# Performance work log

Hardware: AMD Instinct MI355X
Metric: run time of the kernel (lower is better)

The kernel has to match this reference:

```python
import jax, jax.numpy as jnp
import numpy as np

LEVEL_SHAPES = [(100, 134), (50, 67), (25, 34), (13, 17)]  # (H, W) per feature level
NH, NL, NP, D, DFF = 8, 4, 4, 256, 1024
DH = D // NH
LTOT = sum(h * w for h, w in LEVEL_SHAPES)  # 17821
BS, NQ = 4, 300


def _ln(x, w, b):
    m = x.mean(-1, keepdims=True)
    v = ((x - m) ** 2).mean(-1, keepdims=True)
    return (x - m) / jnp.sqrt(v + 1e-5) * w + b


def _mha(q, k, v, in_w, in_b, out_w, out_b):
    B, N, _ = q.shape
    wq, wk, wv = jnp.split(in_w, 3, axis=0)
    bq, bk, bv = jnp.split(in_b, 3)
    qh = (q @ wq.T + bq).reshape(B, N, NH, DH)
    kh = (k @ wk.T + bk).reshape(B, N, NH, DH)
    vh = (v @ wv.T + bv).reshape(B, N, NH, DH)
    a = jax.nn.softmax(jnp.einsum('bqhd,bkhd->bhqk', qh, kh) / float(np.sqrt(DH)), axis=-1)
    o = jnp.einsum('bhqk,bkhd->bqhd', a, vh).reshape(B, N, D)
    return o @ out_w.T + out_b


def _bilinear(img, grid):
    # img [B,C,H,W]; grid [B,N,2] in [-1,1]; align_corners=False, zero padding
    B, C, H, W = img.shape
    x = (grid[..., 0] + 1.0) * 0.5 * W - 0.5
    y = (grid[..., 1] + 1.0) * 0.5 * H - 0.5
    x0f = jnp.floor(x); y0f = jnp.floor(y)
    wx = x - x0f; wy = y - y0f
    x0 = x0f.astype(jnp.int32); y0 = y0f.astype(jnp.int32)
    flat = img.reshape(B, C, H * W)

    def gather(xi, yi):
        m = ((xi >= 0) & (xi < W) & (yi >= 0) & (yi < H)).astype(img.dtype)
        idx = jnp.clip(yi, 0, H - 1) * W + jnp.clip(xi, 0, W - 1)
        g = jnp.take_along_axis(flat, jnp.broadcast_to(idx[:, None, :], (B, C, idx.shape[-1])), axis=2)
        return g * m[:, None, :]

    return (gather(x0, y0) * ((1 - wx) * (1 - wy))[:, None]
            + gather(x0 + 1, y0) * (wx * (1 - wy))[:, None]
            + gather(x0, y0 + 1) * ((1 - wx) * wy)[:, None]
            + gather(x0 + 1, y0 + 1) * (wx * wy)[:, None])


def _msdeform(value, loc, aw):
    # value [B,L,NH,DH]; loc [B,Nq,NH,NL,NP,2] in [0,1]; aw [B,Nq,NH,NL,NP]
    B, Nq = loc.shape[0], loc.shape[1]
    outs = []
    start = 0
    for l, (Hl, Wl) in enumerate(LEVEL_SHAPES):
        v = value[:, start:start + Hl * Wl].transpose(0, 2, 3, 1).reshape(B * NH, DH, Hl, Wl)
        g = (2.0 * loc[:, :, :, l] - 1.0).transpose(0, 2, 1, 3, 4).reshape(B * NH, Nq * NP, 2)
        outs.append(_bilinear(v, g).reshape(B * NH, DH, Nq, NP))
        start += Hl * Wl
    samp = jnp.stack(outs, axis=3)  # [B*NH, DH, Nq, NL, NP]
    w = aw.transpose(0, 2, 1, 3, 4).reshape(B * NH, 1, Nq, NL, NP)
    out = (samp * w).sum(axis=(3, 4))  # [B*NH, DH, Nq]
    return out.reshape(B, NH, DH, Nq).transpose(0, 3, 1, 2).reshape(B, Nq, D)


def _deform_branch(q, ref, src_other, vw, vb, ow, ob, aww, awb, outw, outb):
    B, Nq, _ = q.shape
    value = (src_other @ vw.T + vb).reshape(B, -1, NH, DH)
    off = (q @ ow.T + ob).reshape(B, Nq, NH, NL, NP, 2)
    aw = jax.nn.softmax((q @ aww.T + awb).reshape(B, Nq, NH, NL * NP), axis=-1).reshape(B, Nq, NH, NL, NP)
    norm = jnp.array([[w, h] for h, w in LEVEL_SHAPES], dtype=q.dtype)  # (W,H) per level
    loc = ref[:, :, None, :, None, :] + off / norm[None, None, None, :, None, :]
    return _msdeform(value, loc, aw) @ outw.T + outb


def reference(tgt_RGB, tgt_T, query_pos_RGB, query_pos_T, ref_RGB, ref_T, src_RGB, src_T,
              sa_in_w, sa_in_b, sa_out_w, sa_out_b, ln_w, ln_b,
              ffn_w1, ffn_b1, ffn_w2, ffn_b2,
              val_w, val_b, off_w, off_b, aw_w, aw_b, cout_w, cout_b):
    # --- dual self-attention (eval mode: dropout = identity) ---
    q_RGB = tgt_RGB + query_pos_RGB
    q_T = tgt_T + query_pos_T
    sa_RGB = _mha(q_RGB, q_RGB, tgt_RGB, sa_in_w[0], sa_in_b[0], sa_out_w[0], sa_out_b[0])
    sa_T = _mha(q_T, q_T, tgt_T, sa_in_w[1], sa_in_b[1], sa_out_w[1], sa_out_b[1])
    tgt_RGB = _ln(tgt_RGB + sa_RGB, ln_w[0, 1], ln_b[0, 1])  # norm2_RGB
    tgt_T = _ln(tgt_T + sa_T, ln_w[1, 1], ln_b[1, 1])        # norm2_T
    # --- interactive multi-scale deformable cross-attn: RGB queries sample T memory & vice versa ---
    qc_RGB = tgt_RGB + query_pos_RGB
    qc_T = tgt_T + query_pos_T
    t2_RGB = _deform_branch(qc_RGB, ref_RGB, src_T, val_w[0], val_b[0], off_w[0], off_b[0], aw_w[0], aw_b[0], cout_w[0], cout_b[0])
    t2_T = _deform_branch(qc_T, ref_T, src_RGB, val_w[1], val_b[1], off_w[1], off_b[1], aw_w[1], aw_b[1], cout_w[1], cout_b[1])
    F_RGB, F_T = t2_RGB, t2_T
    # cross residuals exactly as in the torch layer (note the modality swap)
    r = tgt_T + t2_RGB
    t = r + t2_T
    tgt_RGB = _ln(r, ln_w[0, 0], ln_b[0, 0])  # norm1_RGB
    tgt_T = _ln(t, ln_w[1, 0], ln_b[1, 0])    # norm1_T
    # --- FFNs ---
    tgt_RGB = _ln(tgt_RGB + (jax.nn.relu(tgt_RGB @ ffn_w1[0].T + ffn_b1[0]) @ ffn_w2[0].T + ffn_b2[0]), ln_w[0, 2], ln_b[0, 2])
    tgt_T = _ln(tgt_T + (jax.nn.relu(tgt_T @ ffn_w1[1].T + ffn_b1[1]) @ ffn_w2[1].T + ffn_b2[1]), ln_w[1, 2], ln_b[1, 2])
    return tgt_RGB, tgt_T, F_RGB, F_T


def setup_inputs() -> dict:
    key = jax.random.key(0)
    ks = jax.random.split(key, 24)
    s = 0.05
    w = lambda k, shp: jax.random.normal(k, shp, dtype=jnp.float32) * s
    return {
        'tgt_RGB': jax.random.normal(ks[0], (BS, NQ, D), jnp.float32),
        'tgt_T': jax.random.normal(ks[1], (BS, NQ, D), jnp.float32),
        'query_pos_RGB': jax.random.normal(ks[2], (BS, NQ, D), jnp.float32),
        'query_pos_T': jax.random.normal(ks[3], (BS, NQ, D), jnp.float32),
        'ref_RGB': jax.random.uniform(ks[4], (BS, NQ, NL, 2), jnp.float32),
        'ref_T': jax.random.uniform(ks[5], (BS, NQ, NL, 2), jnp.float32),
        'src_RGB': jax.random.normal(ks[6], (BS, LTOT, D), jnp.float32),
        'src_T': jax.random.normal(ks[7], (BS, LTOT, D), jnp.float32),
        'sa_in_w': w(ks[8], (2, 3 * D, D)),
        'sa_in_b': jnp.zeros((2, 3 * D), jnp.float32),
        'sa_out_w': w(ks[9], (2, D, D)),
        'sa_out_b': jnp.zeros((2, D), jnp.float32),
        'ln_w': jnp.ones((2, 3, D), jnp.float32),
        'ln_b': jnp.zeros((2, 3, D), jnp.float32),
        'ffn_w1': w(ks[10], (2, DFF, D)),
        'ffn_b1': jnp.zeros((2, DFF), jnp.float32),
        'ffn_w2': w(ks[11], (2, D, DFF)),
        'ffn_b2': jnp.zeros((2, D), jnp.float32),
        'val_w': w(ks[12], (2, D, D)),
        'val_b': jnp.zeros((2, D), jnp.float32),
        'off_w': w(ks[13], (2, NH * NL * NP * 2, D)),
        'off_b': jax.random.normal(ks[14], (2, NH * NL * NP * 2), jnp.float32) * 0.5,
        'aw_w': w(ks[15], (2, NH * NL * NP, D)),
        'aw_b': jnp.zeros((2, NH * NL * NP), jnp.float32),
        'cout_w': w(ks[16], (2, D, D)),
        'cout_b': jnp.zeros((2, D), jnp.float32),
    }
```

## Files before the change

kernel.cpp:

```cpp
#include <hip/hip_runtime.h>
#include <hip/hip_bf16.h>
#include <cstddef>
#include <math.h>

#define NTOK 1200
#define LTOT_C 17821
#define MVAL 71284
#define STOK (NTOK * 256)

typedef __attribute__((ext_vector_type(8))) short bhalf8;
typedef __attribute__((ext_vector_type(4))) float f32x4;

static __device__ __forceinline__ short f2bf(float f) {
    unsigned u = __builtin_bit_cast(unsigned, f);
    u += 0x7fffu + ((u >> 16) & 1u);
    return (short)(u >> 16);
}
static __device__ __forceinline__ float bf2f(short s) {
    unsigned u = ((unsigned)(unsigned short)s) << 16;
    return __builtin_bit_cast(float, u);
}
static __device__ __forceinline__ bhalf8 cvt8(float4 a, float4 b) {
    bhalf8 h;
    h[0] = f2bf(a.x); h[1] = f2bf(a.y); h[2] = f2bf(a.z); h[3] = f2bf(a.w);
    h[4] = f2bf(b.x); h[5] = f2bf(b.y); h[6] = f2bf(b.z); h[7] = f2bf(b.w);
    return h;
}
static __device__ __forceinline__ void gload_lds16(const void* g, void* l) {
    __builtin_amdgcn_global_load_lds(
        (const __attribute__((address_space(1))) void*)g,
        (__attribute__((address_space(3))) void*)l, 16, 0, 0);
}

struct WcvtArgs { const float* s[10]; short* d[10]; int n[10]; };
__global__ __launch_bounds__(256) void wcvt(WcvtArgs a) {
    const int ti = blockIdx.y;
    const float* s = a.s[ti];
    short* d = a.d[ti];
    const int n = a.n[ti];
    for (int base = (blockIdx.x * 256 + threadIdx.x) * 8; base < n; base += gridDim.x * 256 * 8) {
        const float4 f0 = *reinterpret_cast<const float4*>(s + base);
        const float4 f1 = *reinterpret_cast<const float4*>(s + base + 4);
        *reinterpret_cast<bhalf8*>(d + base) = cvt8(f0, f1);
    }
}

__global__ __launch_bounds__(256) void prep_act(
    const float* __restrict__ tgt0, const float* __restrict__ tgt1,
    const float* __restrict__ pos0, const float* __restrict__ pos1,
    short* __restrict__ qb_bf, short* __restrict__ tgtb,
    const float* __restrict__ off_b, const float* __restrict__ aw_b,
    float* __restrict__ baw)
{
    const int z = blockIdx.y;
    if (blockIdx.x == 0 && z == 0) {
        for (int i = threadIdx.x; i < 768; i += 256) {
            const int zz = i / 384, j = i - zz * 384;
            baw[i] = (j < 256) ? off_b[zz * 256 + j] : aw_b[zz * 128 + (j - 256)];
        }
    }
    const float* tg = z ? tgt1 : tgt0;
    const float* ps = z ? pos1 : pos0;
    const int base = (blockIdx.x * 256 + threadIdx.x) * 8;
    if (base >= STOK) return;
    const float4 t0 = *reinterpret_cast<const float4*>(tg + base);
    const float4 t1 = *reinterpret_cast<const float4*>(tg + base + 4);
    const float4 p0 = *reinterpret_cast<const float4*>(ps + base);
    const float4 p1 = *reinterpret_cast<const float4*>(ps + base + 4);
    float4 s0 = make_float4(t0.x + p0.x, t0.y + p0.y, t0.z + p0.z, t0.w + p0.w);
    float4 s1 = make_float4(t1.x + p1.x, t1.y + p1.y, t1.z + p1.z, t1.w + p1.w);
    *reinterpret_cast<bhalf8*>(qb_bf + (size_t)z * STOK + base) = cvt8(s0, s1);
    *reinterpret_cast<bhalf8*>(tgtb + (size_t)z * STOK + base) = cvt8(t0, t1);
}

__global__ __launch_bounds__(256) void gemm_val(
    const float* __restrict__ A0, const float* __restrict__ A1,
    const short* __restrict__ Wbf, const float* __restrict__ bias,
    short* __restrict__ C)
{
    __shared__ alignas(16) short As[64 * 64];
    __shared__ alignas(16) short Bs[2][128 * 64];
    const int i = blockIdx.x;
    const int widx = (i & 7) * 557 + (i >> 3);
    const int x = widx & 1;
    const int yz = widx >> 1;
    const int z = yz / 1114;
    const int y = yz - z * 1114;
    const float* A = z ? A1 : A0;
    const short* W = Wbf + (size_t)z * 65536;
    const float* bz = bias + z * 256;
    short* Cz = C + (size_t)z * MVAL * 256;
    const int t = threadIdx.x;
    const int wave = t >> 6, lane = t & 63;
    const int l15 = lane & 15, l4 = lane >> 4;
    const int wr = wave >> 1, wc = wave & 1;
    const int bm = y * 64, bn = x * 128;
    f32x4 acc[2][4] = {};

    const int nr8 = lane >> 3, q8 = lane & 7;
    auto stageW = [&](int k0, int buf) {
        #pragma unroll
        for (int ii = 0; ii < 4; ++ii) {
            const int c = wave * 4 + ii;
            const int n = c * 8 + nr8;
            gload_lds16(W + (size_t)(bn + n) * 256 + k0 + ((q8 ^ nr8) << 3),
                        (char*)&Bs[buf][0] + c * 1024);
        }
    };
    float4 paf[2][2];
    auto issueA = [&](int k0) {
        #pragma unroll
        for (int ii = 0; ii < 2; ++ii) {
            const int G = t + ii * 256;
            const int m = G >> 3, g = G & 7;
            const int row = min(bm + m, MVAL - 1);
            const float* s = A + (size_t)row * 256 + k0 + g * 8;
            paf[ii][0] = *reinterpret_cast<const float4*>(s);
            paf[ii][1] = *reinterpret_cast<const float4*>(s + 4);
        }
    };
    auto commitA = [&]() {
        #pragma unroll
        for (int ii = 0; ii < 2; ++ii) {
            const int G = t + ii * 256;
            const int m = G >> 3, g = G & 7;
            *reinterpret_cast<bhalf8*>(&As[m * 64 + ((g ^ (m & 7)) << 3)]) =
                cvt8(paf[ii][0], paf[ii][1]);
        }
    };
    auto compute = [&](int wbuf) {
        #pragma unroll
        for (int kf = 0; kf < 2; ++kf) {
            bhalf8 af[2], bfv[4];
            #pragma unroll
            for (int mf = 0; mf < 2; ++mf) {
                const int m = wr * 32 + (mf << 4) + l15;
                const int g = ((kf << 2) + l4) ^ (m & 7);
                af[mf] = *reinterpret_cast<const bhalf8*>(&As[m * 64 + (g << 3)]);
            }
            #pragma unroll
            for (int nf = 0; nf < 4; ++nf) {
                const int n = (wc << 6) + (nf << 4) + l15;
                const int g = ((kf << 2) + l4) ^ (n & 7);
                bfv[nf] = *reinterpret_cast<const bhalf8*>(&Bs[wbuf][n * 64 + (g << 3)]);
            }
            #pragma unroll
            for (int mf = 0; mf < 2; ++mf)
                #pragma unroll
                for (int nf = 0; nf < 4; ++nf)
                    acc[mf][nf] = __builtin_amdgcn_mfma_f32_16x16x32_bf16(
                        af[mf], bfv[nf], acc[mf][nf], 0, 0, 0);
        }
    };

    issueA(0);
    stageW(0, 0);
    commitA();
    __syncthreads();
    #pragma unroll
    for (int ks = 0; ks < 4; ++ks) {
        const int cur = ks & 1, nxt = cur ^ 1;
        if (ks + 1 < 4) {
            issueA((ks + 1) << 6);
            stageW((ks + 1) << 6, nxt);
        }
        compute(cur);
        if (ks + 1 < 4) {
            __syncthreads();
            commitA();
            __syncthreads();
        }
    }

    float br[4];
    #pragma unroll
    for (int nf = 0; nf < 4; ++nf) br[nf] = bz[bn + (wc << 6) + (nf << 4) + l15];
    #pragma unroll
    for (int mf = 0; mf < 2; ++mf) {
        #pragma unroll
        for (int j = 0; j < 4; ++j) {
            const int row = bm + wr * 32 + (mf << 4) + (l4 << 2) + j;
            if (row >= MVAL) continue;
            const int colbase = bn + (wc << 6);
            #pragma unroll
            for (int nf = 0; nf < 4; ++nf)
                Cz[(size_t)row * 256 + colbase + (nf << 4) + l15] = f2bf(acc[mf][nf][j] + br[nf]);
        }
    }
}

template<bool HASRES, bool RELU, bool OUT_BF16, int BM, int NK>
__global__ __launch_bounds__(256) void gemm_bf16(
    const short* __restrict__ Av, size_t aStrideZ, int lda,
    const short* __restrict__ Wv, size_t wStrideZ, int ldw,
    const float* __restrict__ bias, size_t biasStrideZ,
    const float* __restrict__ Res0, const float* __restrict__ Res1, int ldr,
    void* __restrict__ Cv, size_t cStrideZ, int ldc,
    int M)
{
    constexpr int MFR = BM / 32;
    constexpr int ACW = BM / 32;
    __shared__ alignas(16) short As[2][BM * 64];
    __shared__ alignas(16) short Bs[2][128 * 64];
    const int z = blockIdx.z;
    const short* W = Wv + (size_t)z * wStrideZ;
    const float* bz = bias + (size_t)z * biasStrideZ;
    const int t = threadIdx.x;
    const int wave = t >> 6, lane = t & 63;
    const int l15 = lane & 15, l4 = lane >> 4;
    const int wr = wave >> 1, wc = wave & 1;
    const int bm = blockIdx.y * BM, bn = blockIdx.x * 128;
    f32x4 acc[MFR][4] = {};

    const int nr8 = lane >> 3, q8 = lane & 7;
    auto stageW = [&](int k0, int buf) {
        #pragma unroll
        for (int i = 0; i < 4; ++i) {
            const int c = wave * 4 + i;
            const int n = c * 8 + nr8;
            gload_lds16(W + (size_t)(bn + n) * ldw + k0 + ((q8 ^ nr8) << 3),
                        (char*)&Bs[buf][0] + c * 1024);
        }
    };
    auto stageA = [&](int k0, int buf) {
        #pragma unroll
        for (int i = 0; i < ACW; ++i) {
            const int c = wave * ACW + i;
            const int m = c * 8 + nr8;
            const int row = min(bm + m, M - 1);
            gload_lds16(Av + (size_t)z * aStrideZ + (size_t)row * lda + k0 + ((q8 ^ (m & 7)) << 3),
                        (char*)&As[buf][0] + c * 1024);
        }
    };
    auto compute = [&](int buf) {
        #pragma unroll
        for (int kf = 0; kf < 2; ++kf) {
            bhalf8 af[MFR], bfv[4];
            #pragma unroll
            for (int mf = 0; mf < MFR; ++mf) {
                const int m = wr * (BM / 2) + (mf << 4) + l15;
                const int g = ((kf << 2) + l4) ^ (m & 7);
                af[mf] = *reinterpret_cast<const bhalf8*>(&As[buf][m * 64 + (g << 3)]);
            }
            #pragma unroll
            for (int nf = 0; nf < 4; ++nf) {
                const int n = (wc << 6) + (nf << 4) + l15;
                const int g = ((kf << 2) + l4) ^ (n & 7);
                bfv[nf] = *reinterpret_cast<const bhalf8*>(&Bs[buf][n * 64 + (g << 3)]);
            }
            #pragma unroll
            for (int mf = 0; mf < MFR; ++mf)
                #pragma unroll
                for (int nf = 0; nf < 4; ++nf)
                    acc[mf][nf] = __builtin_amdgcn_mfma_f32_16x16x32_bf16(
                        af[mf], bfv[nf], acc[mf][nf], 0, 0, 0);
        }
    };

    stageA(0, 0);
    stageW(0, 0);
    __syncthreads();
    #pragma unroll
    for (int ks = 0; ks < NK; ++ks) {
        const int cur = ks & 1, nxt = cur ^ 1;
        if (ks + 1 < NK) {
            stageA((ks + 1) << 6, nxt);
            stageW((ks + 1) << 6, nxt);
        }
        compute(cur);
        __syncthreads();
    }

    const float* Rz = HASRES ? (z ? Res1 : Res0) : nullptr;
    float br[4];
    #pragma unroll
    for (int nf = 0; nf < 4; ++nf) br[nf] = bz[bn + (wc << 6) + (nf << 4) + l15];
    #pragma unroll
    for (int mf = 0; mf < MFR; ++mf) {
        #pragma unroll
        for (int j = 0; j < 4; ++j) {
            const int row = bm + wr * (BM / 2) + (mf << 4) + (l4 << 2) + j;
            if (row >= M) continue;
            const int colbase = bn + (wc << 6);
            #pragma unroll
            for (int nf = 0; nf < 4; ++nf) {
                const int col = colbase + (nf << 4) + l15;
                float v = acc[mf][nf][j] + br[nf];
                if (HASRES) v += Rz[(size_t)row * ldr + col];
                if (RELU) v = fmaxf(v, 0.f);
                if (OUT_BF16)
                    ((short*)Cv + (size_t)z * cStrideZ)[(size_t)row * ldc + col] = f2bf(v);
                else
                    ((float*)Cv + (size_t)z * cStrideZ)[(size_t)row * ldc + col] = v;
            }
        }
    }
}

__global__ __launch_bounds__(256) void attn2_kernel(
    const float* __restrict__ qkv_base, short* __restrict__ out_base)
{
    const float scale = 0.17677669529663687f;
    const float* qkv = qkv_base + (size_t)blockIdx.z * 921600;
    short* outp = out_base + (size_t)blockIdx.z * STOK;
    const int b = blockIdx.y >> 3, h = blockIdx.y & 7;
    const int t = threadIdx.x;
    const int ql = t & 31;
    const int kg = t >> 5;
    const int q = blockIdx.x * 32 + ql;
    const bool act = q < 300;
    const float* base = qkv + (size_t)b * 300 * 768;

    float qreg[32];
    if (act) {
        const float4* qp = reinterpret_cast<const float4*>(base + (size_t)q * 768 + h * 32);
        #pragma unroll
        for (int d4 = 0; d4 < 8; ++d4) {
            const float4 v = qp[d4];
            qreg[d4 * 4 + 0] = v.x; qreg[d4 * 4 + 1] = v.y;
            qreg[d4 * 4 + 2] = v.z; qreg[d4 * 4 + 3] = v.w;
        }
    }
    __shared__ float Ks[64][32];
    __shared__ float Vs[64][32];
    float m = -1e30f, l = 0.f, o[32];
    #pragma unroll
    for (int d = 0; d < 32; ++d) o[d] = 0.f;

    for (int k0 = 0; k0 < 300; k0 += 64) {
        const int cnt = min(64, 300 - k0);
        __syncthreads();
        for (int i = t; i < cnt * 32; i += 256) {
            const int kr = i >> 5, d = i & 31;
            Ks[kr][d] = base[(size_t)(k0 + kr) * 768 + 256 + h * 32 + d];
            Vs[kr][d] = base[(size_t)(k0 + kr) * 768 + 512 + h * 32 + d];
        }
        __syncthreads();
        if (act) {
            for (int kk = kg; kk < cnt; kk += 8) {
                const float4* krow = reinterpret_cast<const float4*>(&Ks[kk][0]);
                float s = 0.f;
                #pragma unroll
                for (int d4 = 0; d4 < 8; ++d4) {
                    const float4 kv = krow[d4];
                    s += qreg[d4 * 4 + 0] * kv.x + qreg[d4 * 4 + 1] * kv.y
                       + qreg[d4 * 4 + 2] * kv.z + qreg[d4 * 4 + 3] * kv.w;
                }
                s *= scale;
                const float4* vrow = reinterpret_cast<const float4*>(&Vs[kk][0]);
                if (s <= m) {
                    const float e = __expf(s - m);
                    l += e;
                    #pragma unroll
                    for (int d4 = 0; d4 < 8; ++d4) {
                        const float4 vv = vrow[d4];
                        o[d4 * 4 + 0] += e * vv.x; o[d4 * 4 + 1] += e * vv.y;
                        o[d4 * 4 + 2] += e * vv.z; o[d4 * 4 + 3] += e * vv.w;
                    }
                } else {
                    const float c = __expf(m - s);
                    l = l * c + 1.f;
                    #pragma unroll
                    for (int d4 = 0; d4 < 8; ++d4) {
                        const float4 vv = vrow[d4];
                        o[d4 * 4 + 0] = o[d4 * 4 + 0] * c + vv.x;
                        o[d4 * 4 + 1] = o[d4 * 4 + 1] * c + vv.y;
                        o[d4 * 4 + 2] = o[d4 * 4 + 2] * c + vv.z;
                        o[d4 * 4 + 3] = o[d4 * 4 + 3] * c + vv.w;
                    }
                    m = s;
                }
            }
        }
    }
    __shared__ float pm[32][8];
    __shared__ float pl[32][8];
    __shared__ float po[8][32][33];
    pm[ql][kg] = m; pl[ql][kg] = l;
    #pragma unroll
    for (int d = 0; d < 32; ++d) po[kg][d][ql] = o[d];
    __syncthreads();
    if (kg == 0) {
        float M = pm[ql][0];
        #pragma unroll
        for (int i = 1; i < 8; ++i) M = fmaxf(M, pm[ql][i]);
        float L = 0.f;
        #pragma unroll
        for (int i = 0; i < 8; ++i) L += pl[ql][i] * __expf(pm[ql][i] - M);
        const float invL = 1.f / L;
        #pragma unroll
        for (int i = 0; i < 8; ++i) pm[ql][i] = __expf(pm[ql][i] - M) * invL;
    }
    __syncthreads();
    if (act) {
        #pragma unroll
        for (int dd = 0; dd < 4; ++dd) {
            const int d = kg * 4 + dd;
            float v = 0.f;
            #pragma unroll
            for (int i = 0; i < 8; ++i) v += pm[ql][i] * po[i][d][ql];
            outp[((size_t)b * 300 + q) * 256 + h * 32 + d] = f2bf(v);
        }
    }
}

#define LN_BODY(vexpr, widx)                                                  \
    const int row = blockIdx.x, t = threadIdx.x, z = blockIdx.y;              \
    (void)z;                                                                  \
    const int i = row * 256 + t;                                              \
    const float v = (vexpr);                                                  \
    __shared__ float r1[4], r2[4];                                            \
    float s = v;                                                              \
    _Pragma("unroll")                                                         \
    for (int o = 32; o; o >>= 1) s += __shfl_xor(s, o);                       \
    if ((t & 63) == 0) r1[t >> 6] = s;                                        \
    __syncthreads();                                                          \
    const float mean = (r1[0] + r1[1] + r1[2] + r1[3]) * (1.f / 256.f);       \
    const float dd = v - mean;                                                \
    float sq = dd * dd;                                                       \
    _Pragma("unroll")                                                         \
    for (int o = 32; o; o >>= 1) sq += __shfl_xor(sq, o);                     \
    if ((t & 63) == 0) r2[t >> 6] = sq;                                       \
    __syncthreads();                                                          \
    const float var = (r2[0] + r2[1] + r2[2] + r2[3]) * (1.f / 256.f);        \
    const float y = dd * rsqrtf(var + 1e-5f) * ln_w[(widx) * 256 + t]         \
                    + ln_b[(widx) * 256 + t];

__global__ __launch_bounds__(256) void ln2_fused(
    const float* __restrict__ presum, const float* __restrict__ pos0,
    const float* __restrict__ pos1, const float* __restrict__ ln_w,
    const float* __restrict__ ln_b, short* __restrict__ qc_bf,
    float* __restrict__ tgt2T)
{
    LN_BODY(presum[(size_t)z * STOK + i], z * 3 + 1)
    const float* pos = z ? pos1 : pos0;
    qc_bf[(size_t)z * STOK + i] = f2bf(y + pos[i]);
    if (z == 1) tgt2T[i] = y;
}

__global__ __launch_bounds__(256) void ln1_fused(
    const float* __restrict__ tgt2T, const float* __restrict__ out2,
    const float* __restrict__ out3, const float* __restrict__ ln_w,
    const float* __restrict__ ln_b, short* __restrict__ ln1b,
    float* __restrict__ ln1f)
{
    LN_BODY(tgt2T[row * 256 + t] + out2[row * 256 + t] + (z ? out3[row * 256 + t] : 0.f), z * 3 + 0)
    ln1b[(size_t)z * STOK + i] = f2bf(y);
    ln1f[(size_t)z * STOK + i] = y;
}

__global__ __launch_bounds__(256) void ln3_kernel(
    const float* __restrict__ ffny, const float* __restrict__ ln_w,
    const float* __restrict__ ln_b, float* __restrict__ o0,
    float* __restrict__ o1)
{
    LN_BODY(ffny[(size_t)z * STOK + i], z * 3 + 2)
    (z ? o1 : o0)[i] = y;
}

__global__ __launch_bounds__(256) void sample_kernel(
    const short* __restrict__ valb, const float* __restrict__ oaw,
    const float* __restrict__ ref0, const float* __restrict__ ref1,
    short* __restrict__ out)
{
    const int HL[4] = {100, 50, 25, 13};
    const int WL[4] = {134, 67, 34, 17};
    const int ST[4] = {0, 13400, 16750, 17600};
    const int z = blockIdx.y;
    const int t = threadIdx.x;
    const int wave = t >> 6, lane = t & 63;
    const int qi = wave >> 1, hh = wave & 1;
    const int pp = lane >> 5, h4 = (lane >> 3) & 3, dl = lane & 7;
    const int h = hh * 4 + h4;
    const int bq = blockIdx.x * 2 + qi;
    const int b = bq / 300;
    const float* op = oaw + ((size_t)z * NTOK + bq) * 384;
    const float* offp = op + h * 32;
    const float* awp  = op + 256 + h * 16;
    const float* refp = (z ? ref1 : ref0) + (size_t)bq * 8;
    const short* vb = valb + (size_t)z * MVAL * 256 + (size_t)b * LTOT_C * 256;
    const int co = h * 32 + dl * 4;

    float w16[16];
    float mx = -1e30f;
    #pragma unroll
    for (int i = 0; i < 16; ++i) { w16[i] = awp[i]; mx = fmaxf(mx, w16[i]); }
    float ssum = 0.f;
    #pragma unroll
    for (int i = 0; i < 16; ++i) { w16[i] = __expf(w16[i] - mx); ssum += w16[i]; }
    const float sinv = 1.f / ssum;

    float a0 = 0.f, a1 = 0.f, a2 = 0.f, a3 = 0.f;
#define TAP(cond, ridx, wv)                                                   \
    if (cond) {                                                               \
        const short4 sv = *reinterpret_cast<const short4*>(                   \
            vb + (size_t)(ridx) * 256 + co);                                  \
        a0 += (wv) * bf2f(sv.x); a1 += (wv) * bf2f(sv.y);                     \
        a2 += (wv) * bf2f(sv.z); a3 += (wv) * bf2f(sv.w);                     \
    }
    #pragma unroll
    for (int l = 0; l < 4; ++l) {
        const int Wl = WL[l], Hl = HL[l];
        const float rx = refp[l * 2] * (float)Wl - 0.5f;
        const float ry = refp[l * 2 + 1] * (float)Hl - 0.5f;
        #pragma unroll
        for (int j = 0; j < 2; ++j) {
            const int p = pp * 2 + j;
            const float px = rx + offp[(l * 4 + p) * 2];
            const float py = ry + offp[(l * 4 + p) * 2 + 1];
            const float wgt = w16[l * 4 + p] * sinv;
            const float x0f = floorf(px), y0f = floorf(py);
            const float wx = px - x0f, wy = py - y0f;
            const int x0 = (int)x0f, y0 = (int)y0f;
            const bool xa = (x0 >= 0) & (x0 < Wl);
            const bool xb = (x0 >= -1) & (x0 < Wl - 1);
            const bool ya = (y0 >= 0) & (y0 < Hl);
            const bool yb = (y0 >= -1) & (y0 < Hl - 1);
            const int rbase = ST[l] + y0 * Wl + x0;
            const float w00 = wgt * (1.f - wx) * (1.f - wy);
            const float w10 = wgt * wx * (1.f - wy);
            const float w01 = wgt * (1.f - wx) * wy;
            const float w11 = wgt * wx * wy;
            TAP(ya & xa, rbase, w00)
            TAP(ya & xb, rbase + 1, w10)
            TAP(yb & xa, rbase + Wl, w01)
            TAP(yb & xb, rbase + Wl + 1, w11)
        }
    }
#undef TAP
    a0 += __shfl_xor(a0, 32);
    a1 += __shfl_xor(a1, 32);
    a2 += __shfl_xor(a2, 32);
    a3 += __shfl_xor(a3, 32);
    if (pp == 0) {
        short4 o;
        o.x = f2bf(a0); o.y = f2bf(a1); o.z = f2bf(a2); o.w = f2bf(a3);
        *reinterpret_cast<short4*>(&out[((size_t)z * NTOK + bq) * 256 + co]) = o;
    }
}

extern "C" void kernel_launch(void* const* d_in, const int* in_sizes, int n_in,
                              void* d_out, int out_size, void* d_ws, size_t ws_size,
                              hipStream_t stream) {
    const float* tgt[2] = {(const float*)d_in[0], (const float*)d_in[1]};
    const float* pos[2] = {(const float*)d_in[2], (const float*)d_in[3]};
    const float* ref[2] = {(const float*)d_in[4], (const float*)d_in[5]};
    const float* src[2] = {(const float*)d_in[6], (const float*)d_in[7]};
    const float* sa_in_w  = (const float*)d_in[8];
    const float* sa_in_b  = (const float*)d_in[9];
    const float* sa_out_w = (const float*)d_in[10];
    const float* sa_out_b = (const float*)d_in[11];
    const float* ln_w = (const float*)d_in[12];
    const float* ln_b = (const float*)d_in[13];
    const float* ffn_w1 = (const float*)d_in[14];
    const float* ffn_b1 = (const float*)d_in[15];
    const float* ffn_w2 = (const float*)d_in[16];
    const float* ffn_b2 = (const float*)d_in[17];
    const float* val_w = (const float*)d_in[18];
    const float* val_b = (const float*)d_in[19];
    const float* off_w = (const float*)d_in[20];
    const float* off_b = (const float*)d_in[21];
    const float* aw_w = (const float*)d_in[22];
    const float* aw_b = (const float*)d_in[23];
    const float* cout_w = (const float*)d_in[24];
    const float* cout_b = (const float*)d_in[25];

    char* base = (char*)d_ws;
    size_t off = 0;
    auto alloc = [&](size_t bytes) -> char* {
        char* p = base + off;
        off += (bytes + 255) & ~(size_t)255;
        return p;
    };
    short* wbf   = (short*)alloc((size_t)2031616 * 2);
    float* baw   = (float*)alloc(768 * 4);
    short* qb_bf = (short*)alloc((size_t)2 * STOK * 2);
    short* tgtb  = (short*)alloc((size_t)2 * STOK * 2);
    float* qkv   = (float*)alloc((size_t)2 * 921600 * 4);
    short* attno = (short*)alloc((size_t)2 * STOK * 2);
    float* presum= (float*)alloc((size_t)2 * STOK * 4);
    short* qc_bf = (short*)alloc((size_t)2 * STOK * 2);
    float* tgt2T = (float*)alloc((size_t)STOK * 4);
    float* oawb  = (float*)alloc((size_t)2 * NTOK * 384 * 4);
    short* valb  = (short*)alloc((size_t)2 * MVAL * 256 * 2);
    short* samp  = (short*)alloc((size_t)2 * STOK * 2);
    short* ln1b  = (short*)alloc((size_t)2 * STOK * 2);
    float* ln1f  = (float*)alloc((size_t)2 * STOK * 4);
    short* ffnh  = (short*)alloc((size_t)2 * NTOK * 1024 * 2);
    float* ffny  = (float*)alloc((size_t)2 * STOK * 4);

    short* sa_in_bf  = wbf + 0;
    short* sa_out_bf = wbf + 393216;
    short* ffn1_bf   = wbf + 524288;
    short* ffn2_bf   = wbf + 1048576;
    short* val_bf    = wbf + 1572864;
    short* cout_bf   = wbf + 1703936;
    short* oaw_bf    = wbf + 1835008;

    float* out0 = (float*)d_out;
    float* out1 = out0 + STOK;
    float* out2 = out1 + STOK;
    float* out3 = out2 + STOK;

    const dim3 b256(256);

    WcvtArgs wa;
    wa.s[0] = sa_in_w;        wa.d[0] = sa_in_bf;       wa.n[0] = 393216;
    wa.s[1] = sa_out_w;       wa.d[1] = sa_out_bf;      wa.n[1] = 131072;
    wa.s[2] = ffn_w1;         wa.d[2] = ffn1_bf;        wa.n[2] = 524288;
    wa.s[3] = ffn_w2;         wa.d[3] = ffn2_bf;        wa.n[3] = 524288;
    wa.s[4] = val_w;          wa.d[4] = val_bf;         wa.n[4] = 131072;
    wa.s[5] = cout_w;         wa.d[5] = cout_bf;        wa.n[5] = 131072;
    wa.s[6] = off_w;          wa.d[6] = oaw_bf;         wa.n[6] = 65536;
    wa.s[7] = aw_w;           wa.d[7] = oaw_bf + 65536; wa.n[7] = 32768;
    wa.s[8] = off_w + 65536;  wa.d[8] = oaw_bf + 98304; wa.n[8] = 65536;
    wa.s[9] = aw_w + 32768;   wa.d[9] = oaw_bf + 163840;wa.n[9] = 32768;
    wcvt<<<dim3(128, 10), b256, 0, stream>>>(wa);

    prep_act<<<dim3(150, 2), b256, 0, stream>>>(tgt[0], tgt[1], pos[0], pos[1],
                                                qb_bf, tgtb, off_b, aw_b, baw);

    gemm_val<<<dim3(4456), b256, 0, stream>>>(src[1], src[0], val_bf, val_b, valb);

    gemm_bf16<false, false, false, 64, 4><<<dim3(4, 19, 2), b256, 0, stream>>>(
        qb_bf, (size_t)STOK, 256, sa_in_bf, 196608, 256, sa_in_b, 768,
        nullptr, nullptr, 0, qkv, 921600, 768, NTOK);
    gemm_bf16<false, false, false, 64, 4><<<dim3(2, 19, 2), b256, 0, stream>>>(
        tgtb, (size_t)STOK, 256, sa_in_bf + 512 * 256, 196608, 256, sa_in_b + 512, 768,
        nullptr, nullptr, 0, qkv + 512, 921600, 768, NTOK);

    attn2_kernel<<<dim3(10, 32, 2), b256, 0, stream>>>(qkv, attno);

    gemm_bf16<true, false, false, 64, 4><<<dim3(2, 19, 2), b256, 0, stream>>>(
        attno, (size_t)STOK, 256, sa_out_bf, 65536, 256, sa_out_b, 256,
        tgt[0], tgt[1], 256, presum, (size_t)STOK, 256, NTOK);

    ln2_fused<<<dim3(NTOK, 2), b256, 0, stream>>>(presum, pos[0], pos[1], ln_w, ln_b, qc_bf, tgt2T);

    gemm_bf16<false, false, false, 64, 4><<<dim3(3, 19, 2), b256, 0, stream>>>(
        qc_bf, (size_t)STOK, 256, oaw_bf, 98304, 256, baw, 384,
        nullptr, nullptr, 0, oawb, (size_t)NTOK * 384, 384, NTOK);

    sample_kernel<<<dim3(600, 2), b256, 0, stream>>>(valb, oawb, ref[0], ref[1], samp);

    gemm_bf16<false, false, false, 64, 4><<<dim3(2, 19, 2), b256, 0, stream>>>(
        samp, (size_t)STOK, 256, cout_bf, 65536, 256, cout_b, 256,
        nullptr, nullptr, 0, out2, (size_t)STOK, 256, NTOK);

    ln1_fused<<<dim3(NTOK, 2), b256, 0, stream>>>(tgt2T, out2, out3, ln_w, ln_b, ln1b, ln1f);

    gemm_bf16<false, true, true, 64, 4><<<dim3(8, 19, 2), b256, 0, stream>>>(
        ln1b, (size_t)STOK, 256, ffn1_bf, 262144, 256, ffn_b1, 1024,
        nullptr, nullptr, 0, ffnh, (size_t)NTOK * 1024, 1024, NTOK);

    gemm_bf16<true, false, false, 64, 16><<<dim3(2, 19, 2), b256, 0, stream>>>(
        ffnh, (size_t)NTOK * 1024, 1024, ffn2_bf, 262144, 1024, ffn_b2, 256,
        ln1f, ln1f + STOK, 256, ffny, (size_t)STOK, 256, NTOK);

    ln3_kernel<<<dim3(NTOK, 2), b256, 0, stream>>>(ffny, ln_w, ln_b, out0, out1);
}
```

Baseline: 190.0 us.

## Fuse LayerNorm into output GEMMs, merge QKV launches, narrow value GEMM tiles

Adds a gemm_ln kernel that computes a full 256-wide output row block per workgroup and applies residual add plus LayerNorm in the epilogue. This replaces the sa_out GEMM with ln2_fused and the FFN2 GEMM with ln3_kernel, removing intermediate fp32 buffers and two launches. The two in-projection GEMMs for Q/K and V become one launch, using a second A pointer chosen by blockIdx.x. The value-projection GEMM tile shrinks from 128 to 64 columns, doubling its block count. The fused kernels launch only 38 blocks each, which leaves many CUs idle and risks slower GEMMs.

Measured after the change: 222.7 us. 17.2% more time.

```diff
diff --git a/kernel.cpp b/kernel.cpp
--- a/kernel.cpp
+++ b/kernel.cpp
@@ -79,11 +79,11 @@
     short* __restrict__ C)
 {
     __shared__ alignas(16) short As[64 * 64];
-    __shared__ alignas(16) short Bs[2][128 * 64];
+    __shared__ alignas(16) short Bs[2][64 * 64];
     const int i = blockIdx.x;
-    const int widx = (i & 7) * 557 + (i >> 3);
-    const int x = widx & 1;
-    const int yz = widx >> 1;
+    const int widx = (i & 7) * 1114 + (i >> 3);
+    const int x = widx & 3;
+    const int yz = widx >> 2;
     const int z = yz / 1114;
     const int y = yz - z * 1114;
     const float* A = z ? A1 : A0;
@@ -94,14 +94,14 @@
     const int wave = t >> 6, lane = t & 63;
     const int l15 = lane & 15, l4 = lane >> 4;
     const int wr = wave >> 1, wc = wave & 1;
-    const int bm = y * 64, bn = x * 128;
-    f32x4 acc[2][4] = {};
+    const int bm = y * 64, bn = x * 64;
+    f32x4 acc[2][2] = {};
 
     const int nr8 = lane >> 3, q8 = lane & 7;
     auto stageW = [&](int k0, int buf) {
         #pragma unroll
-        for (int ii = 0; ii < 4; ++ii) {
-            const int c = wave * 4 + ii;
+        for (int ii = 0; ii < 2; ++ii) {
+            const int c = wave * 2 + ii;
             const int n = c * 8 + nr8;
             gload_lds16(W + (size_t)(bn + n) * 256 + k0 + ((q8 ^ nr8) << 3),
                         (char*)&Bs[buf][0] + c * 1024);
@@ -131,7 +131,7 @@
     auto compute = [&](int wbuf) {
         #pragma unroll
         for (int kf = 0; kf < 2; ++kf) {
-            bhalf8 af[2], bfv[4];
+            bhalf8 af[2], bfv[2];
             #pragma unroll
             for (int mf = 0; mf < 2; ++mf) {
                 const int m = wr * 32 + (mf << 4) + l15;
@@ -139,15 +139,15 @@
                 af[mf] = *reinterpret_cast<const bhalf8*>(&As[m * 64 + (g << 3)]);
             }
             #pragma unroll
-            for (int nf = 0; nf < 4; ++nf) {
-                const int n = (wc << 6) + (nf << 4) + l15;
+            for (int nf = 0; nf < 2; ++nf) {
+                const int n = wc * 32 + (nf << 4) + l15;
                 const int g = ((kf << 2) + l4) ^ (n & 7);
                 bfv[nf] = *reinterpret_cast<const bhalf8*>(&Bs[wbuf][n * 64 + (g << 3)]);
             }
             #pragma unroll
             for (int mf = 0; mf < 2; ++mf)
                 #pragma unroll
-                for (int nf = 0; nf < 4; ++nf)
+                for (int nf = 0; nf < 2; ++nf)
                     acc[mf][nf] = __builtin_amdgcn_mfma_f32_16x16x32_bf16(
                         af[mf], bfv[nf], acc[mf][nf], 0, 0, 0);
         }
@@ -172,26 +172,27 @@
         }
     }
 
-    float br[4];
-    #pragma unroll
-    for (int nf = 0; nf < 4; ++nf) br[nf] = bz[bn + (wc << 6) + (nf << 4) + l15];
+    float br[2];
+    #pragma unroll
+    for (int nf = 0; nf < 2; ++nf) br[nf] = bz[bn + wc * 32 + (nf << 4) + l15];
     #pragma unroll
     for (int mf = 0; mf < 2; ++mf) {
         #pragma unroll
         for (int j = 0; j < 4; ++j) {
             const int row = bm + wr * 32 + (mf << 4) + (l4 << 2) + j;
             if (row >= MVAL) continue;
-            const int colbase = bn + (wc << 6);
-            #pragma unroll
-            for (int nf = 0; nf < 4; ++nf)
-                Cz[(size_t)row * 256 + colbase + (nf << 4) + l15] = f2bf(acc[mf][nf][j] + br[nf]);
+            #pragma unroll
+            for (int nf = 0; nf < 2; ++nf)
+                Cz[(size_t)row * 256 + bn + wc * 32 + (nf << 4) + l15] =
+                    f2bf(acc[mf][nf][j] + br[nf]);
         }
     }
 }
 
 template<bool HASRES, bool RELU, bool OUT_BF16, int BM, int NK>
 __global__ __launch_bounds__(256) void gemm_bf16(
-    const short* __restrict__ Av, size_t aStrideZ, int lda,
+    const short* __restrict__ Av, const short* __restrict__ Av2, int xsplit,
+    size_t aStrideZ, int lda,
     const short* __restrict__ Wv, size_t wStrideZ, int ldw,
     const float* __restrict__ bias, size_t biasStrideZ,
     const float* __restrict__ Res0, const float* __restrict__ Res1, int ldr,
@@ -203,6 +204,7 @@
     __shared__ alignas(16) short As[2][BM * 64];
     __shared__ alignas(16) short Bs[2][128 * 64];
     const int z = blockIdx.z;
+    const short* Abase = (Av2 != nullptr && (int)blockIdx.x >= xsplit) ? Av2 : Av;
     const short* W = Wv + (size_t)z * wStrideZ;
     const float* bz = bias + (size_t)z * biasStrideZ;
     const int t = threadIdx.x;
@@ -228,7 +230,7 @@
             const int c = wave * ACW + i;
             const int m = c * 8 + nr8;
             const int row = min(bm + m, M - 1);
-            gload_lds16(Av + (size_t)z * aStrideZ + (size_t)row * lda + k0 + ((q8 ^ (m & 7)) << 3),
+            gload_lds16(Abase + (size_t)z * aStrideZ + (size_t)row * lda + k0 + ((q8 ^ (m & 7)) << 3),
                         (char*)&As[buf][0] + c * 1024);
         }
     };
@@ -292,6 +294,156 @@
                     ((short*)Cv + (size_t)z * cStrideZ)[(size_t)row * ldc + col] = f2bf(v);
                 else
                     ((float*)Cv + (size_t)z * cStrideZ)[(size_t)row * ldc + col] = v;
+            }
+        }
+    }
+}
+
+template<int NK, int MODE>
+__global__ __launch_bounds__(256) void gemm_ln(
+    const short* __restrict__ Av, size_t aStrideZ, int lda,
+    const short* __restrict__ Wv, size_t wStrideZ,
+    const float* __restrict__ bias, size_t biasStrideZ,
+    const float* __restrict__ Res0, const float* __restrict__ Res1,
+    const float* __restrict__ ln_w, const float* __restrict__ ln_b,
+    const float* __restrict__ pos0, const float* __restrict__ pos1,
+    short* __restrict__ qc_bf, float* __restrict__ tgt2T,
+    float* __restrict__ out0, float* __restrict__ out1,
+    int M)
+{
+    __shared__ alignas(16) short As[2][64 * 64];
+    __shared__ alignas(16) short Bs[2][256 * 64];
+    __shared__ float red[2][4][64];
+    const int z = blockIdx.z;
+    const short* W = Wv + (size_t)z * wStrideZ;
+    const float* bz = bias + (size_t)z * biasStrideZ;
+    const float* Rz = z ? Res1 : Res0;
+    const int li = z * 3 + (MODE == 0 ? 1 : 2);
+    const int t = threadIdx.x;
+    const int wave = t >> 6, lane = t & 63;
+    const int l15 = lane & 15, l4 = lane >> 4;
+    const int bm = blockIdx.y * 64;
+    f32x4 acc[4][4] = {};
+
+    const int nr8 = lane >> 3, q8 = lane & 7;
+    auto stageW = [&](int k0, int buf) {
+        #pragma unroll
+        for (int i = 0; i < 8; ++i) {
+            const int c = wave * 8 + i;
+            const int n = c * 8 + nr8;
+            gload_lds16(W + (size_t)n * lda + k0 + ((q8 ^ nr8) << 3),
+                        (char*)&Bs[buf][0] + c * 1024);
+        }
+    };
+    auto stageA = [&](int k0, int buf) {
+        #pragma unroll
+        for (int i = 0; i < 2; ++i) {
+            const int c = wave * 2 + i;
+            const int m = c * 8 + nr8;
+            const int row = min(bm + m, M - 1);
+            gload_lds16(Av + (size_t)z * aStrideZ + (size_t)row * lda + k0 + ((q8 ^ (m & 7)) << 3),
+                        (char*)&As[buf][0] + c * 1024);
+        }
+    };
+    auto compute = [&](int buf) {
+        #pragma unroll
+        for (int kf = 0; kf < 2; ++kf) {
+            bhalf8 af[4], bfv[4];
+            #pragma unroll
+            for (int mf = 0; mf < 4; ++mf) {
+                const int m = (mf << 4) + l15;
+                const int g = ((kf << 2) + l4) ^ (m & 7);
+                af[mf] = *reinterpret_cast<const bhalf8*>(&As[buf][m * 64 + (g << 3)]);
+            }
+            #pragma unroll
+            for (int nf = 0; nf < 4; ++nf) {
+                const int n = (wave << 6) + (nf << 4) + l15;
+                const int g = ((kf << 2) + l4) ^ (n & 7);
+                bfv[nf] = *reinterpret_cast<const bhalf8*>(&Bs[buf][n * 64 + (g << 3)]);
+            }
+            #pragma unroll
+            for (int mf = 0; mf < 4; ++mf)
+                #pragma unroll
+                for (int nf = 0; nf < 4; ++nf)
+                    acc[mf][nf] = __builtin_amdgcn_mfma_f32_16x16x32_bf16(
+                        af[mf], bfv[nf], acc[mf][nf], 0, 0, 0);
+        }
+    };
+
+    stageA(0, 0);
+    stageW(0, 0);
+    __syncthreads();
+    #pragma unroll
+    for (int ks = 0; ks < NK; ++ks) {
+        const int cur = ks & 1, nxt = cur ^ 1;
+        if (ks + 1 < NK) {
+            stageA((ks + 1) << 6, nxt);
+            stageW((ks + 1) << 6, nxt);
+        }
+        compute(cur);
+        __syncthreads();
+    }
+
+    float br[4];
+    #pragma unroll
+    for (int nf = 0; nf < 4; ++nf) br[nf] = bz[(wave << 6) + (nf << 4) + l15];
+    #pragma unroll
+    for (int mf = 0; mf < 4; ++mf) {
+        #pragma unroll
+        for (int j = 0; j < 4; ++j) {
+            const int row = bm + (mf << 4) + (l4 << 2) + j;
+            const int rr = min(row, M - 1);
+            #pragma unroll
+            for (int nf = 0; nf < 4; ++nf) {
+                const int col = (wave << 6) + (nf << 4) + l15;
+                acc[mf][nf][j] += br[nf] + Rz[(size_t)rr * 256 + col];
+            }
+        }
+    }
+    #pragma unroll
+    for (int mf = 0; mf < 4; ++mf) {
+        #pragma unroll
+        for (int j = 0; j < 4; ++j) {
+            float s = 0.f, q = 0.f;
+            #pragma unroll
+            for (int nf = 0; nf < 4; ++nf) {
+                const float v = acc[mf][nf][j];
+                s += v; q += v * v;
+            }
+            #pragma unroll
+            for (int o = 1; o < 16; o <<= 1) {
+                s += __shfl_xor(s, o);
+                q += __shfl_xor(q, o);
+            }
+            if (l15 == 0) {
+                const int rl = (mf << 4) + (l4 << 2) + j;
+                red[0][wave][rl] = s;
+                red[1][wave][rl] = q;
+            }
+        }
+    }
+    __syncthreads();
+    const float* posz = (MODE == 0) ? (z ? pos1 : pos0) : nullptr;
+    #pragma unroll
+    for (int mf = 0; mf < 4; ++mf) {
+        #pragma unroll
+        for (int j = 0; j < 4; ++j) {
+            const int rl = (mf << 4) + (l4 << 2) + j;
+            const int row = bm + rl;
+            if (row >= M) continue;
+            const float mean = (red[0][0][rl] + red[0][1][rl] + red[0][2][rl] + red[0][3][rl]) * (1.f / 256.f);
+            const float ex2  = (red[1][0][rl] + red[1][1][rl] + red[1][2][rl] + red[1][3][rl]) * (1.f / 256.f);
+            const float rstd = rsqrtf(ex2 - mean * mean + 1e-5f);
+            #pragma unroll
+            for (int nf = 0; nf < 4; ++nf) {
+                const int col = (wave << 6) + (nf << 4) + l15;
+                const float yv = (acc[mf][nf][j] - mean) * rstd * ln_w[li * 256 + col] + ln_b[li * 256 + col];
+                if (MODE == 0) {
+                    qc_bf[(size_t)z * STOK + (size_t)row * 256 + col] = f2bf(yv + posz[(size_t)row * 256 + col]);
+                    if (z == 1) tgt2T[(size_t)row * 256 + col] = yv;
+                } else {
+                    (z ? out1 : out0)[(size_t)row * 256 + col] = yv;
+                }
             }
         }
     }
@@ -426,18 +578,6 @@
     const float y = dd * rsqrtf(var + 1e-5f) * ln_w[(widx) * 256 + t]         \
                     + ln_b[(widx) * 256 + t];
 
-__global__ __launch_bounds__(256) void ln2_fused(
-    const float* __restrict__ presum, const float* __restrict__ pos0,
-    const float* __restrict__ pos1, const float* __restrict__ ln_w,
-    const float* __restrict__ ln_b, short* __restrict__ qc_bf,
-    float* __restrict__ tgt2T)
-{
-    LN_BODY(presum[(size_t)z * STOK + i], z * 3 + 1)
-    const float* pos = z ? pos1 : pos0;
-    qc_bf[(size_t)z * STOK + i] = f2bf(y + pos[i]);
-    if (z == 1) tgt2T[i] = y;
-}
-
 __global__ __launch_bounds__(256) void ln1_fused(
     const float* __restrict__ tgt2T, const float* __restrict__ out2,
     const float* __restrict__ out3, const float* __restrict__ ln_w,
@@ -447,15 +587,6 @@
     LN_BODY(tgt2T[row * 256 + t] + out2[row * 256 + t] + (z ? out3[row * 256 + t] : 0.f), z * 3 + 0)
     ln1b[(size_t)z * STOK + i] = f2bf(y);
     ln1f[(size_t)z * STOK + i] = y;
-}
-
-__global__ __launch_bounds__(256) void ln3_kernel(
-    const float* __restrict__ ffny, const float* __restrict__ ln_w,
-    const float* __restrict__ ln_b, float* __restrict__ o0,
-    float* __restrict__ o1)
-{
-    LN_BODY(ffny[(size_t)z * STOK + i], z * 3 + 2)
-    (z ? o1 : o0)[i] = y;
 }
 
 __global__ __launch_bounds__(256) void sample_kernel(
@@ -578,7 +709,6 @@
     short* tgtb  = (short*)alloc((size_t)2 * STOK * 2);
     float* qkv   = (float*)alloc((size_t)2 * 921600 * 4);
     short* attno = (short*)alloc((size_t)2 * STOK * 2);
-    float* presum= (float*)alloc((size_t)2 * STOK * 4);
     short* qc_bf = (short*)alloc((size_t)2 * STOK * 2);
     float* tgt2T = (float*)alloc((size_t)STOK * 4);
     float* oawb  = (float*)alloc((size_t)2 * NTOK * 384 * 4);
@@ -587,7 +717,6 @@
     short* ln1b  = (short*)alloc((size_t)2 * STOK * 2);
     float* ln1f  = (float*)alloc((size_t)2 * STOK * 4);
     short* ffnh  = (short*)alloc((size_t)2 * NTOK * 1024 * 2);
-    float* ffny  = (float*)alloc((size_t)2 * STOK * 4);
 
     short* sa_in_bf  = wbf + 0;
     short* sa_out_bf = wbf + 393216;
@@ -620,42 +749,37 @@
     prep_act<<<dim3(150, 2), b256, 0, stream>>>(tgt[0], tgt[1], pos[0], pos[1],
                                                 qb_bf, tgtb, off_b, aw_b, baw);
 
-    gemm_val<<<dim3(4456), b256, 0, stream>>>(src[1], src[0], val_bf, val_b, valb);
-
-    gemm_bf16<false, false, false, 64, 4><<<dim3(4, 19, 2), b256, 0, stream>>>(
-        qb_bf, (size_t)STOK, 256, sa_in_bf, 196608, 256, sa_in_b, 768,
+    gemm_val<<<dim3(8912), b256, 0, stream>>>(src[1], src[0], val_bf, val_b, valb);
+
+    gemm_bf16<false, false, false, 64, 4><<<dim3(6, 19, 2), b256, 0, stream>>>(
+        qb_bf, tgtb, 4, (size_t)STOK, 256, sa_in_bf, 196608, 256, sa_in_b, 768,
         nullptr, nullptr, 0, qkv, 921600, 768, NTOK);
+
+    attn2_kernel<<<dim3(10, 32, 2), b256, 0, stream>>>(qkv, attno);
+
+    gemm_ln<4, 0><<<dim3(1, 19, 2), b256, 0, stream>>>(
+        attno, (size_t)STOK, 256, sa_out_bf, 65536, sa_out_b, 256,
+        tgt[0], tgt[1], ln_w, ln_b, pos[0], pos[1],
+        qc_bf, tgt2T, nullptr, nullptr, NTOK);
+
+    gemm_bf16<false, false, false, 64, 4><<<dim3(3, 19, 2), b256, 0, stream>>>(
+        qc_bf, nullptr, 1 << 30, (size_t)STOK, 256, oaw_bf, 98304, 256, baw, 384,
+        nullptr, nullptr, 0, oawb, (size_t)NTOK * 384, 384, NTOK);
+
+    sample_kernel<<<dim3(600, 2), b256, 0, stream>>>(valb, oawb, ref[0], ref[1], samp);
+
     gemm_bf16<false, false, false, 64, 4><<<dim3(2, 19, 2), b256, 0, stream>>>(
-        tgtb, (size_t)STOK, 256, sa_in_bf + 512 * 256, 196608, 256, sa_in_b + 512, 768,
-        nullptr, nullptr, 0, qkv + 512, 921600, 768, NTOK);
-
-    attn2_kernel<<<dim3(10, 32, 2), b256, 0, stream>>>(qkv, attno);
-
-    gemm_bf16<true, false, false, 64, 4><<<dim3(2, 19, 2), b256, 0, stream>>>(
-        attno, (size_t)STOK, 256, sa_out_bf, 65536, 256, sa_out_b, 256,
-        tgt[0], tgt[1], 256, presum, (size_t)STOK, 256, NTOK);
-
-    ln2_fused<<<dim3(NTOK, 2), b256, 0, stream>>>(presum, pos[0], pos[1], ln_w, ln_b, qc_bf, tgt2T);
-
-    gemm_bf16<false, false, false, 64, 4><<<dim3(3, 19, 2), b256, 0, stream>>>(
-        qc_bf, (size_t)STOK, 256, oaw_bf, 98304, 256, baw, 384,
-        nullptr, nullptr, 0, oawb, (size_t)NTOK * 384, 384, NTOK);
-
-    sample_kernel<<<dim3(600, 2), b256, 0, stream>>>(valb, oawb, ref[0], ref[1], samp);
-
-    gemm_bf16<false, false, false, 64, 4><<<dim3(2, 19, 2), b256, 0, stream>>>(
-        samp, (size_t)STOK, 256, cout_bf, 65536, 256, cout_b, 256,
+        samp, nullptr, 1 << 30, (size_t)STOK, 256, cout_bf, 65536, 256, cout_b, 256,
         nullptr, nullptr, 0, out2, (size_t)STOK, 256, NTOK);
 
     ln1_fused<<<dim3(NTOK, 2), b256, 0, stream>>>(tgt2T, out2, out3, ln_w, ln_b, ln1b, ln1f);
 
     gemm_bf16<false, true, true, 64, 4><<<dim3(8, 19, 2), b256, 0, stream>>>(
-        ln1b, (size_t)STOK, 256, ffn1_bf, 262144, 256, ffn_b1, 1024,
+        ln1b, nullptr, 1 << 30, (size_t)STOK, 256, ffn1_bf, 262144, 256, ffn_b1, 1024,
         nullptr, nullptr, 0, ffnh, (size_t)NTOK * 1024, 1024, NTOK);
 
-    gemm_bf16<true, false, false, 64, 16><<<dim3(2, 19, 2), b256, 0, stream>>>(
-        ffnh, (size_t)NTOK * 1024, 1024, ffn2_bf, 262144, 1024, ffn_b2, 256,
-        ln1f, ln1f + STOK, 256, ffny, (size_t)STOK, 256, NTOK);
-
-    ln3_kernel<<<dim3(NTOK, 2), b256, 0, stream>>>(ffny, ln_w, ln_b, out0, out1);
-}
+    gemm_ln<16, 1><<<dim3(1, 19, 2), b256, 0, stream>>>(
+        ffnh, (size_t)NTOK * 1024, 1024, ffn2_bf, 262144, ffn_b2, 256,
+        ln1f, ln1f + STOK, ln_w, ln_b, nullptr, nullptr,
+        nullptr, nullptr, out0, out1, NTOK);
+}
```
